# Performance work log

Measured on AMD Instinct MI355X. Metric: run time of the kernel, lower is better.

The kernel has to match this reference:

```python
import jax, jax.numpy as jnp
import numpy as np

D_IN, D_OUT, SEQ = 256, 64, 8192

def setup_inputs() -> dict:
    key = jax.random.key(0)
    kx, kq, kk, kv = jax.random.split(key, 4)
    x = jax.random.normal(kx, (SEQ, D_IN), dtype=jnp.float32)
    # original uses torch.rand (uniform [0,1)) for parameters
    W_q = jax.random.uniform(kq, (D_IN, D_OUT), dtype=jnp.float32)
    W_k = jax.random.uniform(kk, (D_IN, D_OUT), dtype=jnp.float32)
    W_v = jax.random.uniform(kv, (D_IN, D_OUT), dtype=jnp.float32)
    return {"x": x, "W_q": W_q, "W_k": W_k, "W_v": W_v}

def reference(x, W_q, W_k, W_v):
    q = x @ W_q          # [S, d_out]
    k = x @ W_k          # [S, d_out]
    v = x @ W_v          # [S, d_out]
    scores = q @ k.T     # [S, S]
    scale = jnp.asarray(D_OUT, scores.dtype) ** 0.5
    weights = jax.nn.softmax(scores / scale, axis=-1)
    return weights @ v   # [S, d_out]
```

## Files before the change

### kernel.cpp

```cpp
#include <hip/hip_runtime.h>
#include <hip/hip_bf16.h>

#define SEQ   8192
#define DIN   256
#define DOUT  64
#define QSCALE 0.1803368801111204f

using bf16x8 = __attribute__((ext_vector_type(8))) short;
using f32x16 = __attribute__((ext_vector_type(16))) float;

__device__ __forceinline__ float exp2f_fast(float x) { return __builtin_amdgcn_exp2f(x); }
__device__ __forceinline__ f32x16 mfma32(bf16x8 a, bf16x8 b, f32x16 c) {
  return __builtin_amdgcn_mfma_f32_32x32x16_bf16(a, b, c, 0, 0, 0);
}
__device__ __forceinline__ unsigned f2bfbits(float f) {
  unsigned u = __builtin_bit_cast(unsigned, f);
  return (u + 0x7fffu + ((u >> 16) & 1u)) >> 16;
}
__device__ __forceinline__ float bfval(unsigned hb) {
  return __builtin_bit_cast(float, hb << 16);
}
__device__ __forceinline__ unsigned pkb(float a, float b) {
  return f2bfbits(a) | (f2bfbits(b) << 16);
}
__device__ __forceinline__ void gl2lds16(const void* g, void* l) {
  __builtin_amdgcn_global_load_lds(
      (const __attribute__((address_space(1))) unsigned*)g,
      (__attribute__((address_space(3))) unsigned*)l, 16, 0, 0);
}
__device__ __forceinline__ bf16x8 lds_frag(const unsigned short* base, int row, int slot) {
  int phys = slot ^ (row & 7);
  return *(const bf16x8*)&base[row * 64 + phys * 8];
}

__global__ __launch_bounds__(256) void wconv_kernel(
    const float* __restrict__ wq, const float* __restrict__ wk, const float* __restrict__ wv,
    unsigned short* __restrict__ wThi, unsigned short* __restrict__ wTlo)
{
  int flat = blockIdx.x * 256 + threadIdx.x;
  const float* Ws[3] = {wq, wk, wv};
  #pragma unroll
  for (int j = 0; j < 6; ++j) {
    int idx = flat + j * 8192;
    int m = idx >> 14, rem = idx & 16383;
    int c = rem >> 8, d = rem & 255;
    float val = Ws[m][d * 64 + c];
    unsigned hb = f2bfbits(val);
    wThi[idx] = (unsigned short)hb;
    wTlo[idx] = (unsigned short)f2bfbits(val - bfval(hb));
  }
}

__global__ __launch_bounds__(128) void qkv_mfma_kernel(
    const float* __restrict__ x,
    const unsigned short* __restrict__ wThi, const unsigned short* __restrict__ wTlo,
    unsigned short* __restrict__ qhi, unsigned short* __restrict__ qlo,
    unsigned short* __restrict__ khi, unsigned short* __restrict__ klo,
    unsigned short* __restrict__ vThi, unsigned short* __restrict__ vTlo)
{
  const int tid = threadIdx.x, lane = tid & 63, w = tid >> 6;
  const int qr = lane & 31, h = lane >> 5;
  const int mat = blockIdx.y;
  const int r0 = blockIdx.x * 64 + w * 32;

  const unsigned short* wh = &wThi[mat << 14];
  const unsigned short* wl = &wTlo[mat << 14];

  f32x16 acc0, acc1;
  #pragma unroll
  for (int i = 0; i < 16; ++i) { acc0[i] = 0.f; acc1[i] = 0.f; }

  #pragma unroll
  for (int kc = 0; kc < 16; ++kc) {
    const float* xp = &x[(size_t)(r0 + qr) * DIN + kc * 16 + 8 * h];
    float4 xa = *(const float4*)xp;
    float4 xb = *(const float4*)(xp + 4);
    union { unsigned short u[8]; bf16x8 v; } ah, al;
    float xs[8] = {xa.x, xa.y, xa.z, xa.w, xb.x, xb.y, xb.z, xb.w};
    #pragma unroll
    for (int j = 0; j < 8; ++j) {
      unsigned hb = f2bfbits(xs[j]);
      ah.u[j] = (unsigned short)hb;
      al.u[j] = (unsigned short)f2bfbits(xs[j] - bfval(hb));
    }
    bf16x8 bh0 = *(const bf16x8*)&wh[(size_t)(qr)      * DIN + kc * 16 + 8 * h];
    bf16x8 bh1 = *(const bf16x8*)&wh[(size_t)(32 + qr) * DIN + kc * 16 + 8 * h];
    bf16x8 bl0 = *(const bf16x8*)&wl[(size_t)(qr)      * DIN + kc * 16 + 8 * h];
    bf16x8 bl1 = *(const bf16x8*)&wl[(size_t)(32 + qr) * DIN + kc * 16 + 8 * h];
    if (mat < 2) {
      acc0 = mfma32(ah.v, bh0, acc0);
      acc0 = mfma32(al.v, bh0, acc0);
      acc0 = mfma32(ah.v, bl0, acc0);
      acc1 = mfma32(ah.v, bh1, acc1);
      acc1 = mfma32(al.v, bh1, acc1);
      acc1 = mfma32(ah.v, bl1, acc1);
    } else {
      acc0 = mfma32(bh0, ah.v, acc0);
      acc0 = mfma32(bl0, ah.v, acc0);
      acc0 = mfma32(bh0, al.v, acc0);
      acc1 = mfma32(bh1, ah.v, acc1);
      acc1 = mfma32(bl1, ah.v, acc1);
      acc1 = mfma32(bh1, al.v, acc1);
    }
  }

  if (mat < 2) {
    unsigned short* oh = mat ? khi : qhi;
    unsigned short* ol = mat ? klo : qlo;
    const float scale = (mat == 0) ? QSCALE : 1.0f;
    #pragma unroll
    for (int ct = 0; ct < 2; ++ct) {
      const f32x16& A = ct ? acc1 : acc0;
      #pragma unroll
      for (int i = 0; i < 16; ++i) {
        int r = r0 + (i & 3) + 8 * (i >> 2) + 4 * h;
        int c = ct * 32 + qr;
        float val = A[i] * scale;
        unsigned hb = f2bfbits(val);
        oh[(size_t)r * DOUT + c] = (unsigned short)hb;
        ol[(size_t)r * DOUT + c] = (unsigned short)f2bfbits(val - bfval(hb));
      }
    }
  } else {
    #pragma unroll
    for (int ct = 0; ct < 2; ++ct) {
      const f32x16& A = ct ? acc1 : acc0;
      #pragma unroll
      for (int i = 0; i < 16; ++i) {
        int c = ct * 32 + (i & 3) + 8 * (i >> 2) + 4 * h;
        int r = r0 + qr;
        float val = A[i];
        unsigned hb = f2bfbits(val);
        vThi[(size_t)c * SEQ + r] = (unsigned short)hb;
        vTlo[(size_t)c * SEQ + r] = (unsigned short)f2bfbits(val - bfval(hb));
      }
    }
  }
}

__global__ __launch_bounds__(256, 2) void attn_mfma_kernel(
    const unsigned short* __restrict__ qhi, const unsigned short* __restrict__ qlo,
    const unsigned short* __restrict__ khi, const unsigned short* __restrict__ klo,
    const unsigned short* __restrict__ vThi, const unsigned short* __restrict__ vTlo,
    float* __restrict__ opart, float2* __restrict__ mlpart, int slice_len)
{
  __shared__ __align__(1024) unsigned short smx[2][4][4096];
  const int tid  = threadIdx.x;
  const int lane = tid & 63;
  const int w    = tid >> 6;
  const int qr   = lane & 31;
  const int h    = lane >> 5;
  const int split = blockIdx.y;
  const int j0   = split * slice_len;
  const int NT   = slice_len >> 6;
  const int qg0  = blockIdx.x * 256 + w * 64 + qr;
  const int qg1  = qg0 + 32;

  bf16x8 qh0[4], qh1[4];
  #pragma unroll
  for (int c = 0; c < 4; ++c) {
    qh0[c] = *(const bf16x8*)&qhi[(size_t)qg0 * DOUT + c * 16 + 8 * h];
    qh1[c] = *(const bf16x8*)&qhi[(size_t)qg1 * DOUT + c * 16 + 8 * h];
  }

  f32x16 o00, o01, o10, o11;
  #pragma unroll
  for (int i = 0; i < 16; ++i) { o00[i] = 0.f; o01[i] = 0.f; o10[i] = 0.f; o11[i] = 0.f; }
  float m0 = -1.0e30f, m1 = -1.0e30f, l0 = 0.f, l1 = 0.f;

  const int srow_l = lane >> 3;
  const int sslot  = (lane & 7) ^ srow_l;

  auto stage = [&](int t, int nb) {
    const int r0k = j0 + t * 64;
    if (w < 2) {
      const unsigned short* g = (w == 0) ? khi : klo;
      #pragma unroll
      for (int i = 0; i < 8; ++i) {
        int row = 8 * i + srow_l;
        gl2lds16(&g[(size_t)(r0k + row) * DOUT + sslot * 8], &smx[nb][w][i * 512]);
      }
    } else {
      const unsigned short* g = (w == 2) ? vThi : vTlo;
      #pragma unroll
      for (int i = 0; i < 8; ++i) {
        int row = 8 * i + srow_l;
        gl2lds16(&g[(size_t)row * SEQ + r0k + sslot * 8], &smx[nb][w][i * 512]);
      }
    }
  };

  stage(0, 0);
  __syncthreads();

  for (int t = 0; t < NT; ++t) {
    const int b = t & 1;
    if (t + 1 < NT) stage(t + 1, b ^ 1);

    const unsigned short* KH = &smx[b][0][0];
    const unsigned short* KL = &smx[b][1][0];
    const unsigned short* VH = &smx[b][2][0];
    const unsigned short* VL = &smx[b][3][0];

    f32x16 s00, s01, s10, s11;
    #pragma unroll
    for (int i = 0; i < 16; ++i) { s00[i] = 0.f; s01[i] = 0.f; s10[i] = 0.f; s11[i] = 0.f; }
    #pragma unroll
    for (int c = 0; c < 4; ++c) {
      bf16x8 kh0 = lds_frag(KH, qr,      2 * c + h);
      bf16x8 kh1 = lds_frag(KH, qr + 32, 2 * c + h);
      bf16x8 kl0 = lds_frag(KL, qr,      2 * c + h);
      bf16x8 kl1 = lds_frag(KL, qr + 32, 2 * c + h);
      bf16x8 ql0 = *(const bf16x8*)&qlo[(size_t)qg0 * DOUT + c * 16 + 8 * h];
      bf16x8 ql1 = *(const bf16x8*)&qlo[(size_t)qg1 * DOUT + c * 16 + 8 * h];
      s00 = mfma32(kh0, qh0[c], s00);  s01 = mfma32(kh1, qh0[c], s01);
      s10 = mfma32(kh0, qh1[c], s10);  s11 = mfma32(kh1, qh1[c], s11);
      s00 = mfma32(kl0, qh0[c], s00);  s01 = mfma32(kl1, qh0[c], s01);
      s10 = mfma32(kl0, qh1[c], s10);  s11 = mfma32(kl1, qh1[c], s11);
      s00 = mfma32(kh0, ql0, s00);     s01 = mfma32(kh1, ql0, s01);
      s10 = mfma32(kh0, ql1, s10);     s11 = mfma32(kh1, ql1, s11);
    }

    unsigned fw0[4][4], fw1[4][4];
    auto softmax_pack = [&](f32x16& sA, f32x16& sB, f32x16& oA, f32x16& oB,
                            float& mm, float& ll, unsigned fw[4][4]) {
      float pm = sA[0];
      #pragma unroll
      for (int i = 1; i < 16; ++i) pm = fmaxf(pm, sA[i]);
      #pragma unroll
      for (int i = 0; i < 16; ++i) pm = fmaxf(pm, sB[i]);
      pm = fmaxf(pm, __shfl_xor(pm, 32));
      if (__any(pm > mm + 40.0f)) {
        float nm = fmaxf(mm, pm);
        float r = exp2f_fast(mm - nm);
        #pragma unroll
        for (int i = 0; i < 16; ++i) { oA[i] *= r; oB[i] *= r; }
        ll *= r; mm = nm;
      }
      #pragma unroll
      for (int i = 0; i < 16; ++i) sA[i] = exp2f_fast(sA[i] - mm);
      #pragma unroll
      for (int i = 0; i < 16; ++i) sB[i] = exp2f_fast(sB[i] - mm);
      float ls = 0.f;
      #pragma unroll
      for (int i = 0; i < 16; ++i) ls += sA[i] + sB[i];
      ll += ls + __shfl_xor(ls, 32);
      #pragma unroll
      for (int ti = 0; ti < 2; ++ti) {
        #pragma unroll
        for (int c = 0; c < 2; ++c) {
          const f32x16& S = ti ? sB : sA;
          unsigned X0 = pkb(S[8*c+0], S[8*c+1]);
          unsigned Y0 = pkb(S[8*c+2], S[8*c+3]);
          unsigned X1 = pkb(S[8*c+4], S[8*c+5]);
          unsigned Y1 = pkb(S[8*c+6], S[8*c+7]);
          unsigned rX0 = __shfl_xor(X0, 32);
          unsigned rY0 = __shfl_xor(Y0, 32);
          unsigned rX1 = __shfl_xor(X1, 32);
          unsigned rY1 = __shfl_xor(Y1, 32);
          fw[ti*2+c][0] = h ? rX1 : X0;
          fw[ti*2+c][1] = h ? rY1 : Y0;
          fw[ti*2+c][2] = h ? X1  : rX0;
          fw[ti*2+c][3] = h ? Y1  : rY0;
        }
      }
    };
    softmax_pack(s00, s01, o00, o01, m0, l0, fw0);
    softmax_pack(s10, s11, o10, o11, m1, l1, fw1);

    #pragma unroll
    for (int dt = 0; dt < 2; ++dt) {
      f32x16& O0 = dt ? o01 : o00;
      f32x16& O1 = dt ? o11 : o10;
      #pragma unroll
      for (int kc = 0; kc < 4; ++kc) {
        bf16x8 vh = lds_frag(VH, qr + 32 * dt, 2 * kc + h);
        bf16x8 vl = lds_frag(VL, qr + 32 * dt, 2 * kc + h);
        uint4 u0 = {fw0[kc][0], fw0[kc][1], fw0[kc][2], fw0[kc][3]};
        uint4 u1 = {fw1[kc][0], fw1[kc][1], fw1[kc][2], fw1[kc][3]};
        bf16x8 p0 = __builtin_bit_cast(bf16x8, u0);
        bf16x8 p1 = __builtin_bit_cast(bf16x8, u1);
        O0 = mfma32(vh, p0, O0);
        O0 = mfma32(vl, p0, O0);
        O1 = mfma32(vh, p1, O1);
        O1 = mfma32(vl, p1, O1);
      }
    }

    __syncthreads();
  }

  const size_t ob0 = ((size_t)split * SEQ + qg0) * DOUT;
  const size_t ob1 = ((size_t)split * SEQ + qg1) * DOUT;
  #pragma unroll
  for (int b2 = 0; b2 < 4; ++b2) {
    int d0 = 8 * b2 + 4 * h;
    float4 v00 = {o00[4*b2+0], o00[4*b2+1], o00[4*b2+2], o00[4*b2+3]};
    float4 v01 = {o01[4*b2+0], o01[4*b2+1], o01[4*b2+2], o01[4*b2+3]};
    float4 v10 = {o10[4*b2+0], o10[4*b2+1], o10[4*b2+2], o10[4*b2+3]};
    float4 v11 = {o11[4*b2+0], o11[4*b2+1], o11[4*b2+2], o11[4*b2+3]};
    *(float4*)&opart[ob0 + d0]      = v00;
    *(float4*)&opart[ob0 + 32 + d0] = v01;
    *(float4*)&opart[ob1 + d0]      = v10;
    *(float4*)&opart[ob1 + 32 + d0] = v11;
  }
  if (h == 0) {
    mlpart[(size_t)split * SEQ + qg0] = make_float2(m0, l0);
    mlpart[(size_t)split * SEQ + qg1] = make_float2(m1, l1);
  }
}

__global__ __launch_bounds__(256) void combine_kernel(
    const float* __restrict__ opart, const float2* __restrict__ mlpart,
    float* __restrict__ out, int S)
{
  const int tid = threadIdx.x;
  const int row = blockIdx.x * 16 + (tid >> 4);
  const int c4  = tid & 15;
  float mstar = -3.0e38f;
  for (int i = 0; i < S; ++i)
    mstar = fmaxf(mstar, mlpart[(size_t)i * SEQ + row].x);
  float L = 0.f, ax = 0.f, ay = 0.f, az = 0.f, aw = 0.f;
  for (int i = 0; i < S; ++i) {
    float2 ml = mlpart[(size_t)i * SEQ + row];
    float  wgt = exp2f_fast(ml.x - mstar);
    L = fmaf(wgt, ml.y, L);
    float4 ov = ((const float4*)(opart + ((size_t)i * SEQ + row) * DOUT))[c4];
    ax = fmaf(wgt, ov.x, ax); ay = fmaf(wgt, ov.y, ay);
    az = fmaf(wgt, ov.z, az); aw = fmaf(wgt, ov.w, aw);
  }
  float inv = 1.0f / L;
  float4 res = {ax * inv, ay * inv, az * inv, aw * inv};
  ((float4*)(out + (size_t)row * DOUT))[c4] = res;
}

extern "C" void kernel_launch(void* const* d_in, const int* in_sizes, int n_in,
                              void* d_out, int out_size, void* d_ws, size_t ws_size,
                              hipStream_t stream)
{
  const float* x  = (const float*)d_in[0];
  const float* wq = (const float*)d_in[1];
  const float* wk = (const float*)d_in[2];
  const float* wv = (const float*)d_in[3];
  float* out = (float*)d_out;

  char* ws = (char*)d_ws;
  const size_t MB = (size_t)SEQ * DOUT * 2;
  unsigned short* qhi  = (unsigned short*)(ws);
  unsigned short* qlo  = (unsigned short*)(ws + MB);
  unsigned short* khi  = (unsigned short*)(ws + 2 * MB);
  unsigned short* klo  = (unsigned short*)(ws + 3 * MB);
  unsigned short* vThi = (unsigned short*)(ws + 4 * MB);
  unsigned short* vTlo = (unsigned short*)(ws + 5 * MB);
  unsigned short* wThi = (unsigned short*)(ws + 6 * MB);
  unsigned short* wTlo = (unsigned short*)(ws + 6 * MB + 131072);
  float* opart = (float*)(ws + 7 * MB);

  int S = 16;
  while (S > 1) {
    size_t need = 7 * MB + ((size_t)S * SEQ * DOUT + (size_t)S * SEQ * 2) * 4;
    if (need <= ws_size) break;
    S >>= 1;
  }
  float2* mlpart = (float2*)(opart + (size_t)S * SEQ * DOUT);
  const int slice_len = SEQ / S;

  wconv_kernel<<<32, 256, 0, stream>>>(wq, wk, wv, wThi, wTlo);
  qkv_mfma_kernel<<<dim3(SEQ / 64, 3), 128, 0, stream>>>(
      x, wThi, wTlo, qhi, qlo, khi, klo, vThi, vTlo);
  attn_mfma_kernel<<<dim3(SEQ / 256, S), 256, 0, stream>>>(
      qhi, qlo, khi, klo, vThi, vTlo, opart, mlpart, slice_len);
  combine_kernel<<<SEQ / 16, 256, 0, stream>>>(opart, mlpart, out, S);
}
```

Before: 132.4 us.

## Use hardware bf16 pack, hoist q-lo loads, add MFMA priority, remap QKV projection

Replaces software round-to-nearest bf16 conversion with the v_cvt_pk_bf16_f32 instruction in the projection epilogue and the softmax pack. Moves the per-tile global loads of the q low part out of the attention loop into registers before it. Wraps the MFMA sections in s_setprio and changes the max reduction to a pairwise tree. The QKV projection is remapped so each wave computes one 32-column tile for 32 rows, with register prefetch of x and twice as many blocks. This costs more registers in the attention kernel, which could hurt occupancy, and re-reads x per wave in the projection.

```diff
diff --git a/kernel.cpp b/kernel.cpp
--- a/kernel.cpp
+++ b/kernel.cpp
@@ -13,6 +13,11 @@
 __device__ __forceinline__ f32x16 mfma32(bf16x8 a, bf16x8 b, f32x16 c) {
   return __builtin_amdgcn_mfma_f32_32x32x16_bf16(a, b, c, 0, 0, 0);
 }
+__device__ __forceinline__ unsigned cvtpk(float lo, float hi) {
+  unsigned r;
+  asm("v_cvt_pk_bf16_f32 %0, %1, %2" : "=v"(r) : "v"(lo), "v"(hi));
+  return r;
+}
 __device__ __forceinline__ unsigned f2bfbits(float f) {
   unsigned u = __builtin_bit_cast(unsigned, f);
   return (u + 0x7fffu + ((u >> 16) & 1u)) >> 16;
@@ -20,8 +25,11 @@
 __device__ __forceinline__ float bfval(unsigned hb) {
   return __builtin_bit_cast(float, hb << 16);
 }
-__device__ __forceinline__ unsigned pkb(float a, float b) {
-  return f2bfbits(a) | (f2bfbits(b) << 16);
+__device__ __forceinline__ void split2(float a, float b, unsigned& hi, unsigned& lo) {
+  hi = cvtpk(a, b);
+  float ha = __builtin_bit_cast(float, hi << 16);
+  float hb = __builtin_bit_cast(float, hi & 0xffff0000u);
+  lo = cvtpk(a - ha, b - hb);
 }
 __device__ __forceinline__ void gl2lds16(const void* g, void* l) {
   __builtin_amdgcn_global_load_lds(
@@ -58,82 +66,76 @@
     unsigned short* __restrict__ khi, unsigned short* __restrict__ klo,
     unsigned short* __restrict__ vThi, unsigned short* __restrict__ vTlo)
 {
-  const int tid = threadIdx.x, lane = tid & 63, w = tid >> 6;
+  const int tid = threadIdx.x, lane = tid & 63, ct = tid >> 6;
   const int qr = lane & 31, h = lane >> 5;
   const int mat = blockIdx.y;
-  const int r0 = blockIdx.x * 64 + w * 32;
-
-  const unsigned short* wh = &wThi[mat << 14];
-  const unsigned short* wl = &wTlo[mat << 14];
-
-  f32x16 acc0, acc1;
-  #pragma unroll
-  for (int i = 0; i < 16; ++i) { acc0[i] = 0.f; acc1[i] = 0.f; }
-
+  const int r0 = blockIdx.x * 32;
+
+  const unsigned short* wh = &wThi[(mat << 14) + (size_t)(ct * 32) * DIN];
+  const unsigned short* wl = &wTlo[(mat << 14) + (size_t)(ct * 32) * DIN];
+  const float* xrow = &x[(size_t)(r0 + qr) * DIN + 8 * h];
+
+  f32x16 acc;
+  #pragma unroll
+  for (int i = 0; i < 16; ++i) acc[i] = 0.f;
+
+  float4 xa = *(const float4*)&xrow[0];
+  float4 xb = *(const float4*)&xrow[4];
   #pragma unroll
   for (int kc = 0; kc < 16; ++kc) {
-    const float* xp = &x[(size_t)(r0 + qr) * DIN + kc * 16 + 8 * h];
-    float4 xa = *(const float4*)xp;
-    float4 xb = *(const float4*)(xp + 4);
-    union { unsigned short u[8]; bf16x8 v; } ah, al;
-    float xs[8] = {xa.x, xa.y, xa.z, xa.w, xb.x, xb.y, xb.z, xb.w};
-    #pragma unroll
-    for (int j = 0; j < 8; ++j) {
-      unsigned hb = f2bfbits(xs[j]);
-      ah.u[j] = (unsigned short)hb;
-      al.u[j] = (unsigned short)f2bfbits(xs[j] - bfval(hb));
-    }
-    bf16x8 bh0 = *(const bf16x8*)&wh[(size_t)(qr)      * DIN + kc * 16 + 8 * h];
-    bf16x8 bh1 = *(const bf16x8*)&wh[(size_t)(32 + qr) * DIN + kc * 16 + 8 * h];
-    bf16x8 bl0 = *(const bf16x8*)&wl[(size_t)(qr)      * DIN + kc * 16 + 8 * h];
-    bf16x8 bl1 = *(const bf16x8*)&wl[(size_t)(32 + qr) * DIN + kc * 16 + 8 * h];
+    float4 na, nb;
+    if (kc < 15) {
+      na = *(const float4*)&xrow[(kc + 1) * 16];
+      nb = *(const float4*)&xrow[(kc + 1) * 16 + 4];
+    }
+    uint4 hu, lu;
+    split2(xa.x, xa.y, hu.x, lu.x);
+    split2(xa.z, xa.w, hu.y, lu.y);
+    split2(xb.x, xb.y, hu.z, lu.z);
+    split2(xb.z, xb.w, hu.w, lu.w);
+    bf16x8 ah = __builtin_bit_cast(bf16x8, hu);
+    bf16x8 al = __builtin_bit_cast(bf16x8, lu);
+    bf16x8 bh = *(const bf16x8*)&wh[(size_t)qr * DIN + kc * 16 + 8 * h];
+    bf16x8 bl = *(const bf16x8*)&wl[(size_t)qr * DIN + kc * 16 + 8 * h];
     if (mat < 2) {
-      acc0 = mfma32(ah.v, bh0, acc0);
-      acc0 = mfma32(al.v, bh0, acc0);
-      acc0 = mfma32(ah.v, bl0, acc0);
-      acc1 = mfma32(ah.v, bh1, acc1);
-      acc1 = mfma32(al.v, bh1, acc1);
-      acc1 = mfma32(ah.v, bl1, acc1);
+      acc = mfma32(ah, bh, acc);
+      acc = mfma32(al, bh, acc);
+      acc = mfma32(ah, bl, acc);
     } else {
-      acc0 = mfma32(bh0, ah.v, acc0);
-      acc0 = mfma32(bl0, ah.v, acc0);
-      acc0 = mfma32(bh0, al.v, acc0);
-      acc1 = mfma32(bh1, ah.v, acc1);
-      acc1 = mfma32(bl1, ah.v, acc1);
-      acc1 = mfma32(bh1, al.v, acc1);
-    }
+      acc = mfma32(bh, ah, acc);
+      acc = mfma32(bl, ah, acc);
+      acc = mfma32(bh, al, acc);
+    }
+    xa = na; xb = nb;
   }
 
   if (mat < 2) {
     unsigned short* oh = mat ? khi : qhi;
     unsigned short* ol = mat ? klo : qlo;
     const float scale = (mat == 0) ? QSCALE : 1.0f;
-    #pragma unroll
-    for (int ct = 0; ct < 2; ++ct) {
-      const f32x16& A = ct ? acc1 : acc0;
-      #pragma unroll
-      for (int i = 0; i < 16; ++i) {
-        int r = r0 + (i & 3) + 8 * (i >> 2) + 4 * h;
-        int c = ct * 32 + qr;
-        float val = A[i] * scale;
-        unsigned hb = f2bfbits(val);
-        oh[(size_t)r * DOUT + c] = (unsigned short)hb;
-        ol[(size_t)r * DOUT + c] = (unsigned short)f2bfbits(val - bfval(hb));
-      }
+    const int c = ct * 32 + qr;
+    #pragma unroll
+    for (int i = 0; i < 16; i += 2) {
+      float v0 = acc[i] * scale, v1 = acc[i + 1] * scale;
+      unsigned hp, lp;
+      split2(v0, v1, hp, lp);
+      int r = r0 + (i & 3) + 8 * (i >> 2) + 4 * h;
+      oh[(size_t)r * DOUT + c]       = (unsigned short)hp;
+      oh[(size_t)(r + 1) * DOUT + c] = (unsigned short)(hp >> 16);
+      ol[(size_t)r * DOUT + c]       = (unsigned short)lp;
+      ol[(size_t)(r + 1) * DOUT + c] = (unsigned short)(lp >> 16);
     }
   } else {
-    #pragma unroll
-    for (int ct = 0; ct < 2; ++ct) {
-      const f32x16& A = ct ? acc1 : acc0;
-      #pragma unroll
-      for (int i = 0; i < 16; ++i) {
-        int c = ct * 32 + (i & 3) + 8 * (i >> 2) + 4 * h;
-        int r = r0 + qr;
-        float val = A[i];
-        unsigned hb = f2bfbits(val);
-        vThi[(size_t)c * SEQ + r] = (unsigned short)hb;
-        vTlo[(size_t)c * SEQ + r] = (unsigned short)f2bfbits(val - bfval(hb));
-      }
+    const int r = r0 + qr;
+    #pragma unroll
+    for (int i = 0; i < 16; i += 2) {
+      unsigned hp, lp;
+      split2(acc[i], acc[i + 1], hp, lp);
+      int c = ct * 32 + (i & 3) + 8 * (i >> 2) + 4 * h;
+      vThi[(size_t)c * SEQ + r]       = (unsigned short)hp;
+      vThi[(size_t)(c + 1) * SEQ + r] = (unsigned short)(hp >> 16);
+      vTlo[(size_t)c * SEQ + r]       = (unsigned short)lp;
+      vTlo[(size_t)(c + 1) * SEQ + r] = (unsigned short)(lp >> 16);
     }
   }
 }
@@ -156,11 +158,13 @@
   const int qg0  = blockIdx.x * 256 + w * 64 + qr;
   const int qg1  = qg0 + 32;
 
-  bf16x8 qh0[4], qh1[4];
+  bf16x8 qh0[4], qh1[4], qlr0[4], qlr1[4];
   #pragma unroll
   for (int c = 0; c < 4; ++c) {
-    qh0[c] = *(const bf16x8*)&qhi[(size_t)qg0 * DOUT + c * 16 + 8 * h];
-    qh1[c] = *(const bf16x8*)&qhi[(size_t)qg1 * DOUT + c * 16 + 8 * h];
+    qh0[c]  = *(const bf16x8*)&qhi[(size_t)qg0 * DOUT + c * 16 + 8 * h];
+    qh1[c]  = *(const bf16x8*)&qhi[(size_t)qg1 * DOUT + c * 16 + 8 * h];
+    qlr0[c] = *(const bf16x8*)&qlo[(size_t)qg0 * DOUT + c * 16 + 8 * h];
+    qlr1[c] = *(const bf16x8*)&qlo[(size_t)qg1 * DOUT + c * 16 + 8 * h];
   }
 
   f32x16 o00, o01, o10, o11;
@@ -205,30 +209,30 @@
     f32x16 s00, s01, s10, s11;
     #pragma unroll
     for (int i = 0; i < 16; ++i) { s00[i] = 0.f; s01[i] = 0.f; s10[i] = 0.f; s11[i] = 0.f; }
+    __builtin_amdgcn_s_setprio(1);
     #pragma unroll
     for (int c = 0; c < 4; ++c) {
       bf16x8 kh0 = lds_frag(KH, qr,      2 * c + h);
       bf16x8 kh1 = lds_frag(KH, qr + 32, 2 * c + h);
       bf16x8 kl0 = lds_frag(KL, qr,      2 * c + h);
       bf16x8 kl1 = lds_frag(KL, qr + 32, 2 * c + h);
-      bf16x8 ql0 = *(const bf16x8*)&qlo[(size_t)qg0 * DOUT + c * 16 + 8 * h];
-      bf16x8 ql1 = *(const bf16x8*)&qlo[(size_t)qg1 * DOUT + c * 16 + 8 * h];
       s00 = mfma32(kh0, qh0[c], s00);  s01 = mfma32(kh1, qh0[c], s01);
       s10 = mfma32(kh0, qh1[c], s10);  s11 = mfma32(kh1, qh1[c], s11);
       s00 = mfma32(kl0, qh0[c], s00);  s01 = mfma32(kl1, qh0[c], s01);
       s10 = mfma32(kl0, qh1[c], s10);  s11 = mfma32(kl1, qh1[c], s11);
-      s00 = mfma32(kh0, ql0, s00);     s01 = mfma32(kh1, ql0, s01);
-      s10 = mfma32(kh0, ql1, s10);     s11 = mfma32(kh1, ql1, s11);
-    }
+      s00 = mfma32(kh0, qlr0[c], s00); s01 = mfma32(kh1, qlr0[c], s01);
+      s10 = mfma32(kh0, qlr1[c], s10); s11 = mfma32(kh1, qlr1[c], s11);
+    }
+    __builtin_amdgcn_s_setprio(0);
 
     unsigned fw0[4][4], fw1[4][4];
     auto softmax_pack = [&](f32x16& sA, f32x16& sB, f32x16& oA, f32x16& oB,
                             float& mm, float& ll, unsigned fw[4][4]) {
-      float pm = sA[0];
-      #pragma unroll
-      for (int i = 1; i < 16; ++i) pm = fmaxf(pm, sA[i]);
-      #pragma unroll
-      for (int i = 0; i < 16; ++i) pm = fmaxf(pm, sB[i]);
+      float pm = fmaxf(sA[0], sA[1]);
+      #pragma unroll
+      for (int i = 2; i < 16; i += 2) pm = fmaxf(pm, fmaxf(sA[i], sA[i + 1]));
+      #pragma unroll
+      for (int i = 0; i < 16; i += 2) pm = fmaxf(pm, fmaxf(sB[i], sB[i + 1]));
       pm = fmaxf(pm, __shfl_xor(pm, 32));
       if (__any(pm > mm + 40.0f)) {
         float nm = fmaxf(mm, pm);
@@ -250,10 +254,10 @@
         #pragma unroll
         for (int c = 0; c < 2; ++c) {
           const f32x16& S = ti ? sB : sA;
-          unsigned X0 = pkb(S[8*c+0], S[8*c+1]);
-          unsigned Y0 = pkb(S[8*c+2], S[8*c+3]);
-          unsigned X1 = pkb(S[8*c+4], S[8*c+5]);
-          unsigned Y1 = pkb(S[8*c+6], S[8*c+7]);
+          unsigned X0 = cvtpk(S[8*c+0], S[8*c+1]);
+          unsigned Y0 = cvtpk(S[8*c+2], S[8*c+3]);
+          unsigned X1 = cvtpk(S[8*c+4], S[8*c+5]);
+          unsigned Y1 = cvtpk(S[8*c+6], S[8*c+7]);
           unsigned rX0 = __shfl_xor(X0, 32);
           unsigned rY0 = __shfl_xor(Y0, 32);
           unsigned rX1 = __shfl_xor(X1, 32);
@@ -268,6 +272,7 @@
     softmax_pack(s00, s01, o00, o01, m0, l0, fw0);
     softmax_pack(s10, s11, o10, o11, m1, l1, fw1);
 
+    __builtin_amdgcn_s_setprio(1);
     #pragma unroll
     for (int dt = 0; dt < 2; ++dt) {
       f32x16& O0 = dt ? o01 : o00;
@@ -286,6 +291,7 @@
         O1 = mfma32(vl, p1, O1);
       }
     }
+    __builtin_amdgcn_s_setprio(0);
 
     __syncthreads();
   }
@@ -366,7 +372,7 @@
   const int slice_len = SEQ / S;
 
   wconv_kernel<<<32, 256, 0, stream>>>(wq, wk, wv, wThi, wTlo);
-  qkv_mfma_kernel<<<dim3(SEQ / 64, 3), 128, 0, stream>>>(
+  qkv_mfma_kernel<<<dim3(SEQ / 32, 3), 128, 0, stream>>>(
       x, wThi, wTlo, qhi, qlo, khi, klo, vThi, vTlo);
   attn_mfma_kernel<<<dim3(SEQ / 256, S), 256, 0, stream>>>(
       qhi, qlo, khi, klo, vThi, vTlo, opart, mlpart, slice_len);
```

Result: no change. 130.6 us (-1.3%).
